# Optimization experiments

Measured on AMD Instinct MI355X. Metric: run time of the kernel, lower is better.

## Reference

```python
import jax, jax.numpy as jnp
import numpy as np

B, NOBJ = 8192, 1024
EPS = 1e-6


def _euler2rotm(e):
    """e: [..., 3] with (roll, pitch, yaw) on the last dim -> [..., 3, 3] rotation R = RZ @ RY @ RX."""
    roll, pitch, yaw = e[..., 0], e[..., 1], e[..., 2]
    z = jnp.zeros_like(roll)
    o = jnp.ones_like(roll)
    cr, sr = jnp.cos(roll), jnp.sin(roll)
    cp, sp = jnp.cos(pitch), jnp.sin(pitch)
    cy, sy = jnp.cos(yaw), jnp.sin(yaw)
    lead = e.shape[:-1]
    RX = jnp.stack([o, z, z, z, cr, -sr, z, sr, cr], axis=-1).reshape(*lead, 3, 3)
    RY = jnp.stack([cp, z, sp, z, o, z, -sp, z, cp], axis=-1).reshape(*lead, 3, 3)
    RZ = jnp.stack([cy, -sy, z, sy, cy, z, z, z, o], axis=-1).reshape(*lead, 3, 3)
    return jnp.matmul(jnp.matmul(RZ, RY), RX)


def setup_inputs() -> dict:
    key = jax.random.key(0)
    k1, k2 = jax.random.split(key)
    outputs = jax.random.normal(k1, (B, NOBJ, 2, 3), dtype=jnp.float32)
    targets = jax.random.normal(k2, (B, NOBJ, 2, 3), dtype=jnp.float32)
    return {"outputs": outputs, "targets": targets}


def reference(outputs, targets):
    # Module computes a translation loss but immediately overwrites it;
    # only the rotation loss is returned, so only it is computed here.
    src_rot = _euler2rotm(outputs[:, :, 1, :])  # [B, NOBJ, 3, 3]
    tgt_rot = _euler2rotm(targets[:, :, 1, :])  # [B, NOBJ, 3, 3]
    # trace(src @ tgt^T) == elementwise dot of the two matrices
    trace = jnp.sum(src_rot * tgt_rot, axis=(-2, -1))  # [B, NOBJ]
    theta = jnp.clip(0.5 * (trace - 1.0), -1.0 + EPS, 1.0 - EPS)
    rad = jnp.arccos(theta)
    batch = outputs.shape[0]
    return jnp.sum(rad) / batch
```

## Files before the change

kernel.cpp:

```cpp
#include <hip/hip_runtime.h>

#define NPAIRS (8192u * 1024u)
#define BLOCK  256
#define GRID   2048
#define EPSF   1e-6f

__device__ __forceinline__ float pair_loss(float r0, float p0, float y0,
                                           float r1, float p1, float y1) {
    float sr0 = __sinf(r0), cr0 = __cosf(r0);
    float sp0 = __sinf(p0), cp0 = __cosf(p0);
    float sy0 = __sinf(y0), cy0 = __cosf(y0);
    float sr1 = __sinf(r1), cr1 = __cosf(r1);
    float sp1 = __sinf(p1), cp1 = __cosf(p1);
    float sy1 = __sinf(y1), cy1 = __cosf(y1);

    float cysp0 = cy0 * sp0, sysp0 = sy0 * sp0;
    float cysp1 = cy1 * sp1, sysp1 = sy1 * sp1;

    float a00 = cy0 * cp0,               b00 = cy1 * cp1;
    float a01 = cysp0 * sr0 - sy0 * cr0, b01 = cysp1 * sr1 - sy1 * cr1;
    float a02 = cysp0 * cr0 + sy0 * sr0, b02 = cysp1 * cr1 + sy1 * sr1;
    float a10 = sy0 * cp0,               b10 = sy1 * cp1;
    float a11 = sysp0 * sr0 + cy0 * cr0, b11 = sysp1 * sr1 + cy1 * cr1;
    float a12 = sysp0 * cr0 - cy0 * sr0, b12 = sysp1 * cr1 - cy1 * sr1;
    float a20 = -sp0,                    b20 = -sp1;
    float a21 = cp0 * sr0,               b21 = cp1 * sr1;
    float a22 = cp0 * cr0,               b22 = cp1 * cr1;

    float tr = a00 * b00;
    tr = fmaf(a01, b01, tr);
    tr = fmaf(a02, b02, tr);
    tr = fmaf(a10, b10, tr);
    tr = fmaf(a11, b11, tr);
    tr = fmaf(a12, b12, tr);
    tr = fmaf(a20, b20, tr);
    tr = fmaf(a21, b21, tr);
    tr = fmaf(a22, b22, tr);

    float theta = 0.5f * (tr - 1.0f);
    theta = fminf(fmaxf(theta, -1.0f + EPSF), 1.0f - EPSF);
    return acosf(theta);
}

__global__ __launch_bounds__(BLOCK) void rot_loss_partial(
    const float4* __restrict__ outp, const float4* __restrict__ targ,
    float* __restrict__ partial) {
    const unsigned tid = blockIdx.x * BLOCK + threadIdx.x;
    const unsigned nthreads = GRID * BLOCK;
    const unsigned nchunks = NPAIRS / 2;

    float acc = 0.0f;
    for (unsigned i = tid; i < nchunks; i += nthreads) {
        const unsigned base = 3u * i;
        float4 o0 = outp[base + 0];
        float4 o1 = outp[base + 1];
        float4 o2 = outp[base + 2];
        float4 t0 = targ[base + 0];
        float4 t1 = targ[base + 1];
        float4 t2 = targ[base + 2];
        acc += pair_loss(o0.w, o1.x, o1.y, t0.w, t1.x, t1.y);
        acc += pair_loss(o2.y, o2.z, o2.w, t2.y, t2.z, t2.w);
    }

    #pragma unroll
    for (int off = 32; off > 0; off >>= 1) acc += __shfl_down(acc, off);

    __shared__ float ws[BLOCK / 64];
    const int lane = threadIdx.x & 63;
    const int wave = threadIdx.x >> 6;
    if (lane == 0) ws[wave] = acc;
    __syncthreads();
    if (threadIdx.x == 0) {
        float s = 0.0f;
        #pragma unroll
        for (int w = 0; w < BLOCK / 64; ++w) s += ws[w];
        partial[blockIdx.x] = s;
    }
}

__global__ __launch_bounds__(BLOCK) void rot_loss_final(
    const float* __restrict__ partial, float* __restrict__ out) {
    double acc = 0.0;
    for (int i = threadIdx.x; i < GRID; i += BLOCK) acc += (double)partial[i];
    #pragma unroll
    for (int off = 32; off > 0; off >>= 1) acc += __shfl_down(acc, off);
    __shared__ double ws[BLOCK / 64];
    const int lane = threadIdx.x & 63;
    const int wave = threadIdx.x >> 6;
    if (lane == 0) ws[wave] = acc;
    __syncthreads();
    if (threadIdx.x == 0) {
        double s = 0.0;
        #pragma unroll
        for (int w = 0; w < BLOCK / 64; ++w) s += ws[w];
        out[0] = (float)(s / 8192.0);
    }
}

extern "C" void kernel_launch(void* const* d_in, const int* in_sizes, int n_in,
                              void* d_out, int out_size, void* d_ws, size_t ws_size,
                              hipStream_t stream) {
    const float4* outp = (const float4*)d_in[0];
    const float4* targ = (const float4*)d_in[1];
    float* partial = (float*)d_ws;
    float* out = (float*)d_out;

    rot_loss_partial<<<GRID, BLOCK, 0, stream>>>(outp, targ, partial);
    rot_loss_final<<<1, BLOCK, 0, stream>>>(partial, out);
}
```

Before: 392.3 us.

## Simplify rotation trace with angle differences and prefetch next chunk loads

Rewrites the trace of the two ZYX rotation matrices in closed form using roll and yaw differences. This cuts the sin/cos evaluations per pair from twelve to eight and replaces most of the matrix-building arithmetic. It also software-pipelines the grid-stride loop so the loads for the next chunk are issued before the current one is computed, hiding memory latency at the cost of extra registers. The new formula changes floating-point rounding slightly, and its correctness depends on the algebraic identity holding.

```diff
diff --git a/kernel.cpp b/kernel.cpp
--- a/kernel.cpp
+++ b/kernel.cpp
@@ -7,37 +7,20 @@
 
 __device__ __forceinline__ float pair_loss(float r0, float p0, float y0,
                                            float r1, float p1, float y1) {
-    float sr0 = __sinf(r0), cr0 = __cosf(r0);
     float sp0 = __sinf(p0), cp0 = __cosf(p0);
-    float sy0 = __sinf(y0), cy0 = __cosf(y0);
-    float sr1 = __sinf(r1), cr1 = __cosf(r1);
     float sp1 = __sinf(p1), cp1 = __cosf(p1);
-    float sy1 = __sinf(y1), cy1 = __cosf(y1);
+    float dr = r1 - r0, dy = y1 - y0;
+    float sdr = __sinf(dr), cdr = __cosf(dr);
+    float sdy = __sinf(dy), cdy = __cosf(dy);
 
-    float cysp0 = cy0 * sp0, sysp0 = sy0 * sp0;
-    float cysp1 = cy1 * sp1, sysp1 = sy1 * sp1;
+    float m2 = sp0 * sp1;
+    float cc = cdr * cdy;
+    float tr = cp0 * cp1 * (cdr + cdy);
+    tr += m2;
+    tr += fmaf(m2, cc, cc);
+    tr = fmaf(sp0 + sp1, sdr * sdy, tr);
 
-    float a00 = cy0 * cp0,               b00 = cy1 * cp1;
-    float a01 = cysp0 * sr0 - sy0 * cr0, b01 = cysp1 * sr1 - sy1 * cr1;
-    float a02 = cysp0 * cr0 + sy0 * sr0, b02 = cysp1 * cr1 + sy1 * sr1;
-    float a10 = sy0 * cp0,               b10 = sy1 * cp1;
-    float a11 = sysp0 * sr0 + cy0 * cr0, b11 = sysp1 * sr1 + cy1 * cr1;
-    float a12 = sysp0 * cr0 - cy0 * sr0, b12 = sysp1 * cr1 - cy1 * sr1;
-    float a20 = -sp0,                    b20 = -sp1;
-    float a21 = cp0 * sr0,               b21 = cp1 * sr1;
-    float a22 = cp0 * cr0,               b22 = cp1 * cr1;
-
-    float tr = a00 * b00;
-    tr = fmaf(a01, b01, tr);
-    tr = fmaf(a02, b02, tr);
-    tr = fmaf(a10, b10, tr);
-    tr = fmaf(a11, b11, tr);
-    tr = fmaf(a12, b12, tr);
-    tr = fmaf(a20, b20, tr);
-    tr = fmaf(a21, b21, tr);
-    tr = fmaf(a22, b22, tr);
-
-    float theta = 0.5f * (tr - 1.0f);
+    float theta = fmaf(0.5f, tr, -0.5f);
     theta = fminf(fmaxf(theta, -1.0f + EPSF), 1.0f - EPSF);
     return acosf(theta);
 }
@@ -50,16 +33,27 @@
     const unsigned nchunks = NPAIRS / 2;
 
     float acc = 0.0f;
-    for (unsigned i = tid; i < nchunks; i += nthreads) {
-        const unsigned base = 3u * i;
-        float4 o0 = outp[base + 0];
-        float4 o1 = outp[base + 1];
-        float4 o2 = outp[base + 2];
-        float4 t0 = targ[base + 0];
-        float4 t1 = targ[base + 1];
-        float4 t2 = targ[base + 2];
+    unsigned i = tid;
+    unsigned b = 3u * i;
+    float4 o0 = outp[b], o1 = outp[b + 1], o2 = outp[b + 2];
+    float4 t0 = targ[b], t1 = targ[b + 1], t2 = targ[b + 2];
+
+    #pragma unroll 1
+    for (;;) {
+        const unsigned inext = i + nthreads;
+        const bool more = inext < nchunks;
+        float4 no0, no1, no2, nt0, nt1, nt2;
+        if (more) {
+            const unsigned nb = 3u * inext;
+            no0 = outp[nb]; no1 = outp[nb + 1]; no2 = outp[nb + 2];
+            nt0 = targ[nb]; nt1 = targ[nb + 1]; nt2 = targ[nb + 2];
+        }
         acc += pair_loss(o0.w, o1.x, o1.y, t0.w, t1.x, t1.y);
         acc += pair_loss(o2.y, o2.z, o2.w, t2.y, t2.z, t2.w);
+        if (!more) break;
+        o0 = no0; o1 = no1; o2 = no2;
+        t0 = nt0; t1 = nt1; t2 = nt2;
+        i = inext;
     }
 
     #pragma unroll
```

New measurement: 389.9 us. About the same (-0.6%).
